# Kernel tuning notes

Measured on AMD Instinct MI355X. Metric: run time of the kernel, lower is better.

The kernel has to match this reference:

```python
import jax, jax.numpy as jnp
import numpy as np

GMO_SIGMA = 1.0
EPS_GMO = 1e-16
EPS_BARY = 1e-16
EPS_DIV = 1e-12
CHUNK = 512  # points per search chunk to bound [B, CHUNK, F] intermediates


def _tri_sqdist(p, a, b, c):
    """Exact squared point-to-triangle distance (Ericson).
    p: [B,Pc,1,3], a/b/c: [B,1,F,3] -> [B,Pc,F]"""
    ab = b - a
    ac = c - a
    ap = p - a
    d1 = (ab * ap).sum(-1)
    d2 = (ac * ap).sum(-1)
    bp = p - b
    d3 = (ab * bp).sum(-1)
    d4 = (ac * bp).sum(-1)
    cp_ = p - c
    d5 = (ab * cp_).sum(-1)
    d6 = (ac * cp_).sum(-1)
    va = d3 * d6 - d5 * d4
    vb = d5 * d2 - d1 * d6
    vc = d1 * d4 - d3 * d2
    # candidate closest points per region
    t_ab = d1 / jnp.maximum(d1 - d3, EPS_DIV)
    t_ac = d2 / jnp.maximum(d2 - d6, EPS_DIV)
    t_bc = (d4 - d3) / jnp.maximum((d4 - d3) + (d5 - d6), EPS_DIV)
    den = jnp.maximum(va + vb + vc, EPS_DIV)
    v = (vb / den)[..., None]
    w = (vc / den)[..., None]
    cp = a + v * ab + w * ac  # face interior (default)
    m_bc = (va <= 0) & ((d4 - d3) >= 0) & ((d5 - d6) >= 0)
    m_ac = (vb <= 0) & (d2 >= 0) & (d6 <= 0)
    m_ab = (vc <= 0) & (d1 >= 0) & (d3 <= 0)
    m_a = (d1 <= 0) & (d2 <= 0)
    m_b = (d3 >= 0) & (d4 <= d3)
    m_c = (d6 >= 0) & (d5 <= d6)
    cp = jnp.where(m_bc[..., None], b + t_bc[..., None] * (c - b), cp)
    cp = jnp.where(m_ac[..., None], a + t_ac[..., None] * ac, cp)
    cp = jnp.where(m_ab[..., None], a + t_ab[..., None] * ab, cp)
    cp = jnp.where(m_c[..., None], c, cp)
    cp = jnp.where(m_b[..., None], b, cp)
    cp = jnp.where(m_a[..., None], a, cp)
    return ((p - cp) ** 2).sum(-1)


def _nearest_face_idx(points, tri):
    """points: [B,P,3], tri: [B,F,3,3] -> int32 [B,P] index of nearest face."""
    B, P, _ = points.shape
    a = tri[:, None, :, 0, :]
    b = tri[:, None, :, 1, :]
    c = tri[:, None, :, 2, :]
    nC = P // CHUNK
    pts = points.reshape(B, nC, CHUNK, 3).transpose(1, 0, 2, 3)  # [nC,B,Pc,3]

    def chunk_fn(p):  # p: [B,Pc,3]
        d = _tri_sqdist(p[:, :, None, :], a, b, c)  # [B,Pc,F]
        return jnp.argmin(d, axis=-1)

    idx = jax.lax.map(chunk_fn, pts)  # [nC,B,Pc]
    return idx.transpose(1, 0, 2).reshape(B, P)


def _barycentric(a, b, c, q):
    v1 = b - a
    v2 = c - a
    n = jnp.cross(v1, v2)
    n_dot_n = (n * n).sum(-1)
    n_dot_n = jnp.where(n_dot_n < EPS_BARY, 1.0, n_dot_n)
    w = q - a
    gamma = (jnp.cross(v1, w) * n).sum(-1) / n_dot_n
    beta = (jnp.cross(w, v2) * n).sum(-1) / n_dot_n
    alpha = 1.0 - beta - gamma
    return jnp.stack((alpha, beta, gamma), axis=-1)


def _gmo(sqr_input, sigma):
    sqr_sigma = sigma ** 2
    return jnp.sqrt(sqr_sigma * (sqr_input / (sqr_sigma + sqr_input)) + EPS_GMO)


def setup_inputs() -> dict:
    key = jax.random.key(0)
    k1, k2, k3 = jax.random.split(key, 3)
    points = jax.random.normal(k1, (2, 2048, 3), dtype=jnp.float32)
    mesh_vertices = jax.random.normal(k2, (2, 2562, 3), dtype=jnp.float32)
    mesh_faces = jax.random.randint(k3, (5120, 3), 0, 2562, dtype=jnp.int32)
    return {"points": points, "mesh_vertices": mesh_vertices, "mesh_faces": mesh_faces}


def reference(points, mesh_vertices, mesh_faces):
    B, P, _ = points.shape
    tri = mesh_vertices[:, mesh_faces]  # [B,F,3,3] face vertices
    face_idx = _nearest_face_idx(points, tri)  # [B,P]
    closest_tri = jnp.take_along_axis(tri, face_idx[:, :, None, None], axis=1)  # [B,P,3,3]
    a = closest_tri[:, :, 0, :]
    b = closest_tri[:, :, 1, :]
    c = closest_tri[:, :, 2, :]
    bco = _barycentric(a, b, c, points)  # [B,P,3]
    closest_points = (a * bco[:, :, 0:1] + b * bco[:, :, 1:2] + c * bco[:, :, 2:3])
    square_distances = ((closest_points - points) ** 2).sum(-1)
    robust = _gmo(square_distances, GMO_SIGMA)
    return robust.mean(-1).mean()
```

## Files before the change

### kernel.cpp

```cpp
#include <hip/hip_runtime.h>
#include <math.h>

#define EPS_GMO  1e-16f
#define EPS_BARY 1e-16f
#define EPS_DIV  1e-12f
#define TPB  512
#define RTPB 256
#define NWAVE (TPB / 64)
#define GPTS 4
#define FSTRIDE 12
#define QCAP 2048
#define NFK 12

__global__ void gather_fdat_kernel(const float* __restrict__ verts,
                                   const int* __restrict__ faces,
                                   float* __restrict__ fdat,
                                   int B, int F, int V)
{
    int i = blockIdx.x * blockDim.x + threadIdx.x;
    if (i >= B * F) return;
    int b = i / F;
    int f = i - b * F;
    int i0 = faces[f * 3 + 0], i1 = faces[f * 3 + 1], i2 = faces[f * 3 + 2];
    const float* pa = verts + ((size_t)b * V + i0) * 3;
    const float* pb = verts + ((size_t)b * V + i1) * 3;
    const float* pc = verts + ((size_t)b * V + i2) * 3;
    float ax = pa[0], ay = pa[1], az = pa[2];
    float abx = pb[0] - ax, aby = pb[1] - ay, abz = pb[2] - az;
    float acx = pc[0] - ax, acy = pc[1] - ay, acz = pc[2] - az;
    float saa = abx * abx + aby * aby + abz * abz;
    float sab = abx * acx + aby * acy + abz * acz;
    float scc = acx * acx + acy * acy + acz * acz;
    float* o = fdat + (size_t)i * FSTRIDE;
    o[0] = ax;  o[1] = ay;  o[2] = az;
    o[3] = abx; o[4] = aby; o[5] = abz;
    o[6] = acx; o[7] = acy; o[8] = acz;
    o[9] = saa; o[10] = sab; o[11] = scc;
}

__device__ float tri_sqdist_exact(float px, float py, float pz,
                                  float ax, float ay, float az,
                                  float bx, float by, float bz,
                                  float cx, float cy, float cz)
{
#pragma clang fp contract(off)
    float abx = bx - ax, aby = by - ay, abz = bz - az;
    float acx = cx - ax, acy = cy - ay, acz = cz - az;
    float apx = px - ax, apy = py - ay, apz = pz - az;
    float d1 = abx * apx + aby * apy + abz * apz;
    float d2 = acx * apx + acy * apy + acz * apz;
    float bpx = px - bx, bpy = py - by, bpz = pz - bz;
    float d3 = abx * bpx + aby * bpy + abz * bpz;
    float d4 = acx * bpx + acy * bpy + acz * bpz;
    float cpx_ = px - cx, cpy_ = py - cy, cpz_ = pz - cz;
    float d5 = abx * cpx_ + aby * cpy_ + abz * cpz_;
    float d6 = acx * cpx_ + acy * cpy_ + acz * cpz_;
    float va = d3 * d6 - d5 * d4;
    float vb = d5 * d2 - d1 * d6;
    float vc = d1 * d4 - d3 * d2;
    float t_ab = d1 / fmaxf(d1 - d3, EPS_DIV);
    float t_ac = d2 / fmaxf(d2 - d6, EPS_DIV);
    float t_bc = (d4 - d3) / fmaxf((d4 - d3) + (d5 - d6), EPS_DIV);
    float den = fmaxf(va + vb + vc, EPS_DIV);
    float v = vb / den;
    float w = vc / den;
    float qx = ax + v * abx + w * acx;
    float qy = ay + v * aby + w * acy;
    float qz = az + v * abz + w * acz;
    bool m_bc = (va <= 0.0f) && (d4 - d3 >= 0.0f) && (d5 - d6 >= 0.0f);
    bool m_ac = (vb <= 0.0f) && (d2 >= 0.0f) && (d6 <= 0.0f);
    bool m_ab = (vc <= 0.0f) && (d1 >= 0.0f) && (d3 <= 0.0f);
    bool m_a  = (d1 <= 0.0f) && (d2 <= 0.0f);
    bool m_b  = (d3 >= 0.0f) && (d4 <= d3);
    bool m_c  = (d6 >= 0.0f) && (d5 <= d6);
    if (m_bc) { qx = bx + t_bc * (cx - bx); qy = by + t_bc * (cy - by); qz = bz + t_bc * (cz - bz); }
    if (m_ac) { qx = ax + t_ac * acx;       qy = ay + t_ac * acy;       qz = az + t_ac * acz; }
    if (m_ab) { qx = ax + t_ab * abx;       qy = ay + t_ab * aby;       qz = az + t_ab * abz; }
    if (m_c)  { qx = cx; qy = cy; qz = cz; }
    if (m_b)  { qx = bx; qy = by; qz = bz; }
    if (m_a)  { qx = ax; qy = ay; qz = az; }
    float dx = px - qx, dy = py - qy, dz = pz - qz;
    return dx * dx + dy * dy + dz * dz;
}

__global__ __launch_bounds__(TPB) void p2s_main_kernel(
    const float* __restrict__ points,
    const float* __restrict__ verts,
    const int* __restrict__ faces,
    const float* __restrict__ fdat,
    float* __restrict__ robust_out,
    int P, int V, int F, int npts)
{
    __shared__ float swmin[NWAVE][GPTS];
    __shared__ float sargd[NWAVE][GPTS];
    __shared__ int   sargi[NWAVE][GPTS];
    __shared__ int   sFace[GPTS];
    __shared__ unsigned squeue[QCAP];
    __shared__ unsigned scnt;

    const int tid  = threadIdx.x;
    const int lane = tid & 63;
    const int wid  = tid >> 6;
    const int gp0  = blockIdx.x * GPTS;
    const int b    = gp0 / P;

    if (tid == 0) scnt = 0;

    float px[GPTS], py[GPTS], pz[GPTS];
#pragma unroll
    for (int g = 0; g < GPTS; ++g) {
        int gp = gp0 + g; if (gp >= npts) gp = npts - 1;
        const float* pp = points + (size_t)gp * 3;
        px[g] = pp[0]; py[g] = pp[1]; pz[g] = pp[2];
    }

    const float* fb = fdat + (size_t)b * F * FSTRIDE;

    float dfast[NFK][GPTS];
    float best[GPTS];
#pragma unroll
    for (int g = 0; g < GPTS; ++g) best[g] = INFINITY;
#pragma unroll
    for (int k = 0; k < NFK; ++k)
#pragma unroll
        for (int g = 0; g < GPTS; ++g) dfast[k][g] = INFINITY;

#pragma unroll
    for (int k = 0; k < NFK; ++k) {
        int f = tid + k * TPB;
        if (f >= F) break;
        const float* fd = fb + (size_t)f * FSTRIDE;
        float4 q0 = *(const float4*)(fd + 0);
        float4 q1 = *(const float4*)(fd + 4);
        float4 q2 = *(const float4*)(fd + 8);
        float ax = q0.x, ay = q0.y, az = q0.z;
        float abx = q0.w, aby = q1.x, abz = q1.y;
        float acx = q1.z, acy = q1.w, acz = q2.x;
        float saa = q2.y, sab = q2.z, scc = q2.w;
        float cbb = saa - 2.0f * sab + scc;
        float det = saa * scc - sab * sab;
        float rsaa = __builtin_amdgcn_rcpf(fmaxf(saa, 1e-30f));
        float rscc = __builtin_amdgcn_rcpf(fmaxf(scc, 1e-30f));
        float rcbb = __builtin_amdgcn_rcpf(fmaxf(cbb, 1e-30f));
        float rdet = __builtin_amdgcn_rcpf(fmaxf(det, 1e-30f));
        float k1 = saa - sab;
#pragma unroll
        for (int g = 0; g < GPTS; ++g) {
            float apx = px[g] - ax, apy = py[g] - ay, apz = pz[g] - az;
            float sap = apx * apx + apy * apy + apz * apz;
            float d1 = apx * abx + apy * aby + apz * abz;
            float d2 = apx * acx + apy * acy + apz * acz;
            float t0 = __builtin_amdgcn_fmed3f(d1 * rsaa, 0.0f, 1.0f);
            float h0 = d1 + d1;
            float dab = sap - t0 * (h0 - t0 * saa);
            float t1 = __builtin_amdgcn_fmed3f(d2 * rscc, 0.0f, 1.0f);
            float dac = sap - t1 * ((d2 + d2) - t1 * scc);
            float e1 = (d2 - d1) + k1;
            float t2 = __builtin_amdgcn_fmed3f(e1 * rcbb, 0.0f, 1.0f);
            float bpp = (sap - h0) + saa;
            float dbc = bpp - t2 * ((e1 + e1) - t2 * cbb);
            float dmin = fminf(fminf(dab, dac), dbc);
            float vnum = scc * d1 - sab * d2;
            float wnum = saa * d2 - sab * d1;
            bool inside = (vnum >= 0.0f) & (wnum >= 0.0f) & ((vnum + wnum) <= det);
            float idist = sap - (vnum * d1 + wnum * d2) * rdet;
            float d = fmaxf(inside ? fminf(idist, dmin) : dmin, 0.0f);
            dfast[k][g] = d;
            best[g] = fminf(best[g], d);
        }
    }

#pragma unroll
    for (int m = 1; m < 64; m <<= 1) {
#pragma unroll
        for (int g = 0; g < GPTS; ++g)
            best[g] = fminf(best[g], __shfl_xor(best[g], m));
    }
    if (lane == 0) {
#pragma unroll
        for (int g = 0; g < GPTS; ++g) swmin[wid][g] = best[g];
    }
    __syncthreads();

    float Tg[GPTS];
#pragma unroll
    for (int g = 0; g < GPTS; ++g) {
        float mn = swmin[0][g];
#pragma unroll
        for (int w = 1; w < NWAVE; ++w) mn = fminf(mn, swmin[w][g]);
        Tg[g] = mn + (1e-4f + 1e-2f * mn);
    }

#pragma unroll
    for (int k = 0; k < NFK; ++k) {
        int f = tid + k * TPB;
        if (f >= F) break;
#pragma unroll
        for (int g = 0; g < GPTS; ++g) {
            if (dfast[k][g] <= Tg[g]) {
                unsigned idx = atomicAdd(&scnt, 1u);
                if (idx < QCAP) squeue[idx] = ((unsigned)g << 13) | (unsigned)f;
            }
        }
    }
    __syncthreads();
    unsigned total = scnt;

    float bestE[GPTS]; int bestI[GPTS];
#pragma unroll
    for (int g = 0; g < GPTS; ++g) { bestE[g] = INFINITY; bestI[g] = 0x7fffffff; }

    if (total <= QCAP) {
        for (unsigned q = tid; q < total; q += TPB) {
            unsigned e = squeue[q];
            int g = (int)(e >> 13);
            int f = (int)(e & 0x1fffu);
            int i0 = faces[f * 3 + 0], i1 = faces[f * 3 + 1], i2 = faces[f * 3 + 2];
            const float* pa = verts + ((size_t)b * V + i0) * 3;
            const float* pbv = verts + ((size_t)b * V + i1) * 3;
            const float* pc = verts + ((size_t)b * V + i2) * 3;
            float de = tri_sqdist_exact(px[g], py[g], pz[g],
                                        pa[0], pa[1], pa[2],
                                        pbv[0], pbv[1], pbv[2],
                                        pc[0], pc[1], pc[2]);
            if (de < bestE[g] || (de == bestE[g] && f < bestI[g])) {
                bestE[g] = de; bestI[g] = f;
            }
        }
    } else {
#pragma unroll
        for (int k = 0; k < NFK; ++k) {
            int f = tid + k * TPB;
            if (f >= F) break;
            bool any = false;
#pragma unroll
            for (int g = 0; g < GPTS; ++g) any = any || (dfast[k][g] <= Tg[g]);
            if (any) {
                int i0 = faces[f * 3 + 0], i1 = faces[f * 3 + 1], i2 = faces[f * 3 + 2];
                const float* pa = verts + ((size_t)b * V + i0) * 3;
                const float* pbv = verts + ((size_t)b * V + i1) * 3;
                const float* pc = verts + ((size_t)b * V + i2) * 3;
                float ax = pa[0], ay = pa[1], az = pa[2];
                float bx = pbv[0], by = pbv[1], bz = pbv[2];
                float cx = pc[0], cy = pc[1], cz = pc[2];
#pragma unroll
                for (int g = 0; g < GPTS; ++g) {
                    if (dfast[k][g] <= Tg[g]) {
                        float de = tri_sqdist_exact(px[g], py[g], pz[g],
                                                    ax, ay, az, bx, by, bz, cx, cy, cz);
                        if (de < bestE[g]) { bestE[g] = de; bestI[g] = f; }
                    }
                }
            }
        }
    }

#pragma unroll
    for (int m = 1; m < 64; m <<= 1) {
#pragma unroll
        for (int g = 0; g < GPTS; ++g) {
            float od = __shfl_xor(bestE[g], m);
            int   oi = __shfl_xor(bestI[g], m);
            if (od < bestE[g] || (od == bestE[g] && oi < bestI[g])) {
                bestE[g] = od; bestI[g] = oi;
            }
        }
    }
    if (lane == 0) {
#pragma unroll
        for (int g = 0; g < GPTS; ++g) { sargd[wid][g] = bestE[g]; sargi[wid][g] = bestI[g]; }
    }
    __syncthreads();

    if (tid == 0) {
#pragma unroll
        for (int g = 0; g < GPTS; ++g) {
            float dmn = sargd[0][g]; int imn = sargi[0][g];
#pragma unroll
            for (int w = 1; w < NWAVE; ++w) {
                float dv = sargd[w][g]; int iv = sargi[w][g];
                if (dv < dmn || (dv == dmn && iv < imn)) { dmn = dv; imn = iv; }
            }
            sFace[g] = imn;
        }
    }
    __syncthreads();

    if (tid < GPTS) {
#pragma clang fp contract(off)
        int g = tid;
        int gp = gp0 + g;
        if (gp < npts) {
            int f = sFace[g];
            int i0 = faces[f * 3 + 0], i1 = faces[f * 3 + 1], i2 = faces[f * 3 + 2];
            const float* pa = verts + ((size_t)b * V + i0) * 3;
            const float* pbv = verts + ((size_t)b * V + i1) * 3;
            const float* pc = verts + ((size_t)b * V + i2) * 3;
            float ax = pa[0], ay = pa[1], az = pa[2];
            float bx = pbv[0], by = pbv[1], bz = pbv[2];
            float cx = pc[0], cy = pc[1], cz = pc[2];
            float Px = px[g], Py = py[g], Pz = pz[g];
            float v1x = bx - ax, v1y = by - ay, v1z = bz - az;
            float v2x = cx - ax, v2y = cy - ay, v2z = cz - az;
            float nx = v1y * v2z - v1z * v2y;
            float ny = v1z * v2x - v1x * v2z;
            float nz = v1x * v2y - v1y * v2x;
            float nn = nx * nx + ny * ny + nz * nz;
            if (nn < EPS_BARY) nn = 1.0f;
            float wx = Px - ax, wy = Py - ay, wz = Pz - az;
            float c1x = v1y * wz - v1z * wy;
            float c1y = v1z * wx - v1x * wz;
            float c1z = v1x * wy - v1y * wx;
            float gamma = (c1x * nx + c1y * ny + c1z * nz) / nn;
            float c2x = wy * v2z - wz * v2y;
            float c2y = wz * v2x - wx * v2z;
            float c2z = wx * v2y - wy * v2x;
            float beta = (c2x * nx + c2y * ny + c2z * nz) / nn;
            float alpha = 1.0f - beta - gamma;
            float cpx = ax * alpha + bx * beta + cx * gamma;
            float cpy = ay * alpha + by * beta + cy * gamma;
            float cpz = az * alpha + bz * beta + cz * gamma;
            float dx = cpx - Px, dy = cpy - Py, dz = cpz - Pz;
            float sdist = dx * dx + dy * dy + dz * dz;
            float r = sqrtf(sdist / (1.0f + sdist) + EPS_GMO);
            robust_out[gp] = r;
        }
    }
}

__global__ __launch_bounds__(RTPB) void reduce_mean_kernel(
    const float* __restrict__ vals, float* __restrict__ out, int N, float inv)
{
    __shared__ float s[RTPB];
    int tid = threadIdx.x;
    float acc = 0.0f;
    for (int i = tid; i < N; i += RTPB) acc += vals[i];
    s[tid] = acc;
    __syncthreads();
    for (int st = RTPB / 2; st > 0; st >>= 1) {
        if (tid < st) s[tid] += s[tid + st];
        __syncthreads();
    }
    if (tid == 0) out[0] = s[0] * inv;
}

extern "C" void kernel_launch(void* const* d_in, const int* in_sizes, int n_in,
                              void* d_out, int out_size, void* d_ws, size_t ws_size,
                              hipStream_t stream)
{
    const float* points = (const float*)d_in[0];
    const float* verts  = (const float*)d_in[1];
    const int*   faces  = (const int*)d_in[2];
    float* out = (float*)d_out;

    const int B = 2;
    const int P = in_sizes[0] / (B * 3);
    const int V = in_sizes[1] / (B * 3);
    const int F = in_sizes[2] / 3;
    const int npts = B * P;

    float* fdat   = (float*)d_ws;
    float* robust = fdat + (size_t)B * F * FSTRIDE;

    int nBF = B * F;
    gather_fdat_kernel<<<(nBF + RTPB - 1) / RTPB, RTPB, 0, stream>>>(verts, faces, fdat, B, F, V);

    int nBlocks = (npts + GPTS - 1) / GPTS;
    p2s_main_kernel<<<nBlocks, TPB, 0, stream>>>(points, verts, faces, fdat, robust, P, V, F, npts);

    reduce_mean_kernel<<<1, RTPB, 0, stream>>>(robust, out, npts, 1.0f / (float)npts);
}
```

Baseline: 58.68 us.

## Store quantized per-face distance codes in LDS instead of register array

The 48-entry per-thread register array of fast distances is replaced by an 8-bit monotone code per point (exponent plus two mantissa bits), packed four to a word. The packed words go into dynamic shared memory indexed by face, and the face loops become runtime-strided loops. The aim is to cut VGPR pressure and raise occupancy, and a barrier is removed by folding the final cross-wave argmin into the per-point epilogue. The coarse quantization makes the candidate filter looser, so more faces may go through the exact distance check. It also adds about F*4 bytes of LDS per block.

New measurement: 53.31 us (median of 2 runs). 1.1x faster.

```diff
diff --git a/kernel.cpp b/kernel.cpp
--- a/kernel.cpp
+++ b/kernel.cpp
@@ -10,7 +10,6 @@
 #define GPTS 4
 #define FSTRIDE 12
 #define QCAP 2048
-#define NFK 12
 
 __global__ void gather_fdat_kernel(const float* __restrict__ verts,
                                    const int* __restrict__ faces,
@@ -83,6 +82,13 @@
     return dx * dx + dy * dy + dz * dz;
 }
 
+__device__ __forceinline__ int dcode(float d)
+{
+    unsigned raw = __float_as_uint(d) >> 21;
+    int c = (int)raw - 380;
+    return c < 0 ? 0 : (c > 255 ? 255 : c);
+}
+
 __global__ __launch_bounds__(TPB) void p2s_main_kernel(
     const float* __restrict__ points,
     const float* __restrict__ verts,
@@ -91,10 +97,10 @@
     float* __restrict__ robust_out,
     int P, int V, int F, int npts)
 {
+    extern __shared__ unsigned dstore32[];
     __shared__ float swmin[NWAVE][GPTS];
     __shared__ float sargd[NWAVE][GPTS];
     __shared__ int   sargi[NWAVE][GPTS];
-    __shared__ int   sFace[GPTS];
     __shared__ unsigned squeue[QCAP];
     __shared__ unsigned scnt;
 
@@ -116,19 +122,11 @@
 
     const float* fb = fdat + (size_t)b * F * FSTRIDE;
 
-    float dfast[NFK][GPTS];
     float best[GPTS];
 #pragma unroll
     for (int g = 0; g < GPTS; ++g) best[g] = INFINITY;
-#pragma unroll
-    for (int k = 0; k < NFK; ++k)
-#pragma unroll
-        for (int g = 0; g < GPTS; ++g) dfast[k][g] = INFINITY;
-
-#pragma unroll
-    for (int k = 0; k < NFK; ++k) {
-        int f = tid + k * TPB;
-        if (f >= F) break;
+
+    for (int f = tid; f < F; f += TPB) {
         const float* fd = fb + (size_t)f * FSTRIDE;
         float4 q0 = *(const float4*)(fd + 0);
         float4 q1 = *(const float4*)(fd + 4);
@@ -144,6 +142,7 @@
         float rcbb = __builtin_amdgcn_rcpf(fmaxf(cbb, 1e-30f));
         float rdet = __builtin_amdgcn_rcpf(fmaxf(det, 1e-30f));
         float k1 = saa - sab;
+        unsigned wcode = 0;
 #pragma unroll
         for (int g = 0; g < GPTS; ++g) {
             float apx = px[g] - ax, apy = py[g] - ay, apz = pz[g] - az;
@@ -165,9 +164,10 @@
             bool inside = (vnum >= 0.0f) & (wnum >= 0.0f) & ((vnum + wnum) <= det);
             float idist = sap - (vnum * d1 + wnum * d2) * rdet;
             float d = fmaxf(inside ? fminf(idist, dmin) : dmin, 0.0f);
-            dfast[k][g] = d;
+            wcode |= (unsigned)dcode(d) << (8 * g);
             best[g] = fminf(best[g], d);
         }
+        dstore32[f] = wcode;
     }
 
 #pragma unroll
@@ -182,22 +182,21 @@
     }
     __syncthreads();
 
-    float Tg[GPTS];
+    float Tg[GPTS]; int codeT[GPTS];
 #pragma unroll
     for (int g = 0; g < GPTS; ++g) {
         float mn = swmin[0][g];
 #pragma unroll
         for (int w = 1; w < NWAVE; ++w) mn = fminf(mn, swmin[w][g]);
         Tg[g] = mn + (1e-4f + 1e-2f * mn);
-    }
-
-#pragma unroll
-    for (int k = 0; k < NFK; ++k) {
-        int f = tid + k * TPB;
-        if (f >= F) break;
+        codeT[g] = dcode(Tg[g]);
+    }
+
+    for (int f = tid; f < F; f += TPB) {
+        unsigned w = dstore32[f];
 #pragma unroll
         for (int g = 0; g < GPTS; ++g) {
-            if (dfast[k][g] <= Tg[g]) {
+            if ((int)((w >> (8 * g)) & 0xffu) <= codeT[g]) {
                 unsigned idx = atomicAdd(&scnt, 1u);
                 if (idx < QCAP) squeue[idx] = ((unsigned)g << 13) | (unsigned)f;
             }
@@ -228,13 +227,14 @@
             }
         }
     } else {
-#pragma unroll
-        for (int k = 0; k < NFK; ++k) {
-            int f = tid + k * TPB;
-            if (f >= F) break;
-            bool any = false;
-#pragma unroll
-            for (int g = 0; g < GPTS; ++g) any = any || (dfast[k][g] <= Tg[g]);
+        for (int f = tid; f < F; f += TPB) {
+            unsigned w = dstore32[f];
+            bool cg[GPTS]; bool any = false;
+#pragma unroll
+            for (int g = 0; g < GPTS; ++g) {
+                cg[g] = (int)((w >> (8 * g)) & 0xffu) <= codeT[g];
+                any = any || cg[g];
+            }
             if (any) {
                 int i0 = faces[f * 3 + 0], i1 = faces[f * 3 + 1], i2 = faces[f * 3 + 2];
                 const float* pa = verts + ((size_t)b * V + i0) * 3;
@@ -245,7 +245,7 @@
                 float cx = pc[0], cy = pc[1], cz = pc[2];
 #pragma unroll
                 for (int g = 0; g < GPTS; ++g) {
-                    if (dfast[k][g] <= Tg[g]) {
+                    if (cg[g]) {
                         float de = tri_sqdist_exact(px[g], py[g], pz[g],
                                                     ax, ay, az, bx, by, bz, cx, cy, cz);
                         if (de < bestE[g]) { bestE[g] = de; bestI[g] = f; }
@@ -272,26 +272,18 @@
     }
     __syncthreads();
 
-    if (tid == 0) {
-#pragma unroll
-        for (int g = 0; g < GPTS; ++g) {
-            float dmn = sargd[0][g]; int imn = sargi[0][g];
-#pragma unroll
-            for (int w = 1; w < NWAVE; ++w) {
-                float dv = sargd[w][g]; int iv = sargi[w][g];
-                if (dv < dmn || (dv == dmn && iv < imn)) { dmn = dv; imn = iv; }
-            }
-            sFace[g] = imn;
-        }
-    }
-    __syncthreads();
-
     if (tid < GPTS) {
 #pragma clang fp contract(off)
         int g = tid;
+        float dmn = sargd[0][g]; int imn = sargi[0][g];
+#pragma unroll
+        for (int w = 1; w < NWAVE; ++w) {
+            float dv = sargd[w][g]; int iv = sargi[w][g];
+            if (dv < dmn || (dv == dmn && iv < imn)) { dmn = dv; imn = iv; }
+        }
+        int f = imn;
         int gp = gp0 + g;
         if (gp < npts) {
-            int f = sFace[g];
             int i0 = faces[f * 3 + 0], i1 = faces[f * 3 + 1], i2 = faces[f * 3 + 2];
             const float* pa = verts + ((size_t)b * V + i0) * 3;
             const float* pbv = verts + ((size_t)b * V + i1) * 3;
@@ -366,7 +358,8 @@
     gather_fdat_kernel<<<(nBF + RTPB - 1) / RTPB, RTPB, 0, stream>>>(verts, faces, fdat, B, F, V);
 
     int nBlocks = (npts + GPTS - 1) / GPTS;
-    p2s_main_kernel<<<nBlocks, TPB, 0, stream>>>(points, verts, faces, fdat, robust, P, V, F, npts);
+    size_t dynLds = (size_t)F * sizeof(unsigned);
+    p2s_main_kernel<<<nBlocks, TPB, dynLds, stream>>>(points, verts, faces, fdat, robust, P, V, F, npts);
 
     reduce_mean_kernel<<<1, RTPB, 0, stream>>>(robust, out, npts, 1.0f / (float)npts);
 }
```
